# Optimization experiments

Measured on AMD Instinct MI355X. Metric: run time of the kernel, lower is better.

Reference implementation:

```python
import jax, jax.numpy as jnp
import numpy as np

N, T, C, K = 32, 1024, 512, 64
EPS = 1e-12  # torch F.normalize eps


def _l2norm(v, axis):
    n = jnp.sqrt(jnp.sum(v * v, axis=axis, keepdims=True))
    return v / jnp.maximum(n, EPS)


def setup_inputs() -> dict:
    key = jax.random.key(0)
    k1, k2 = jax.random.split(key)
    x = jax.random.normal(k1, (N, T, C), dtype=jnp.float32)
    centroids = jax.random.uniform(k2, (K, C), dtype=jnp.float32)
    # mirrors _init_params: conv.weight = 0.2*centroids, conv.bias = -0.1*||centroids||
    W = 0.2 * centroids
    b = -0.1 * jnp.sqrt(jnp.sum(centroids * centroids, axis=1))
    return {"x": x, "W": W, "b": b, "centroids": centroids}


def reference(x, W, b, centroids):
    # x: [N, T, C] -> [N, C, T]
    xt = jnp.transpose(x, (0, 2, 1))
    # 1x1 Conv1d == per-timestep linear: logits [N, K, T]
    logits = jnp.einsum('kc,nct->nkt', W, xt) + b[None, :, None]
    a = jax.nn.softmax(logits, axis=1)  # softmax over clusters
    # vlad[n,k,c] = sum_t a[n,k,t] * (x[n,c,t] - centroid[k,c])
    #            = (a @ x^T) - sum_t(a) * centroid  (GEMM form, same math)
    vlad = jnp.einsum('nkt,nct->nkc', a, xt) - a.sum(axis=-1)[:, :, None] * centroids[None]
    vlad = _l2norm(vlad, axis=2)          # intra-normalization per cluster
    vlad = vlad.reshape(vlad.shape[0], -1)
    vlad = _l2norm(vlad, axis=1)          # global L2 normalization
    return vlad
```

## Files before the change

kernel.cpp:

```cpp
#include <hip/hip_runtime.h>
#include <cmath>

namespace {

constexpr int N = 32, T = 1024, C = 512, K = 64;
constexpr float EPS = 1e-12f;

typedef short s8v __attribute__((ext_vector_type(8)));
typedef short s4v __attribute__((ext_vector_type(4)));
typedef short s2v __attribute__((ext_vector_type(2)));
typedef float f4v __attribute__((ext_vector_type(4)));

__device__ inline unsigned short f2bh(float f) {
  __bf16 h = (__bf16)f;
  return __builtin_bit_cast(unsigned short, h);
}
__device__ inline float bh2f(unsigned short u) {
  __bf16 h = __builtin_bit_cast(__bf16, u);
  return (float)h;
}

#define MFMA16(A, B, Cc) __builtin_amdgcn_mfma_f32_16x16x32_bf16((A), (B), (Cc), 0, 0, 0)

__global__ __launch_bounds__(256, 4) void k_gemm1(
    const float* __restrict__ x, const float* __restrict__ W,
    const float* __restrict__ b, float* __restrict__ aT,
    float* __restrict__ asum_part) {
  __shared__ __align__(16) unsigned short sm[4 * 64 * 72];
  __shared__ float asum_l[256];
  unsigned short* xh_s = sm;
  unsigned short* xl_s = sm + 64 * 72;
  unsigned short* wh_s = sm + 2 * 64 * 72;
  unsigned short* wl_s = sm + 3 * 64 * 72;

  const int tid = threadIdx.x;
  const int w = tid >> 6, lane = tid & 63, lm = lane & 15, lq = lane >> 4;
  const int th = w >> 1;
  const int kh = w & 1;
  const long r0 = (long)blockIdx.x * 64;
  const int n = blockIdx.x >> 4, tl = blockIdx.x & 15;

  f4v acc[2][2] = {};
  float4 px[4], pw[4];
#pragma unroll
  for (int r = 0; r < 4; ++r) {
    const int f = tid + r * 256, t = f >> 4, cg = f & 15;
    px[r] = *(const float4*)&x[(r0 + t) * C + cg * 4];
    pw[r] = *(const float4*)&W[(long)t * C + cg * 4];
  }

  for (int c0 = 0; c0 < C; c0 += 64) {
    __syncthreads();
#pragma unroll
    for (int r = 0; r < 4; ++r) {
      const int f = tid + r * 256, t = f >> 4, cg = f & 15;
      const float ex[4] = {px[r].x, px[r].y, px[r].z, px[r].w};
      const float ew[4] = {pw[r].x, pw[r].y, pw[r].z, pw[r].w};
      s4v xh, xl, wh, wl;
#pragma unroll
      for (int i = 0; i < 4; ++i) {
        unsigned short hb = f2bh(ex[i]);
        xh[i] = (short)hb; xl[i] = (short)f2bh(ex[i] - bh2f(hb));
        hb = f2bh(ew[i]);
        wh[i] = (short)hb; wl[i] = (short)f2bh(ew[i] - bh2f(hb));
      }
      *(s4v*)&xh_s[t * 72 + cg * 4] = xh;
      *(s4v*)&xl_s[t * 72 + cg * 4] = xl;
      *(s4v*)&wh_s[t * 72 + cg * 4] = wh;
      *(s4v*)&wl_s[t * 72 + cg * 4] = wl;
    }
    __syncthreads();
    if (c0 + 64 < C) {
#pragma unroll
      for (int r = 0; r < 4; ++r) {
        const int f = tid + r * 256, t = f >> 4, cg = f & 15;
        px[r] = *(const float4*)&x[(r0 + t) * C + c0 + 64 + cg * 4];
        pw[r] = *(const float4*)&W[(long)t * C + c0 + 64 + cg * 4];
      }
    }

#pragma unroll
    for (int ks = 0; ks < 2; ++ks) {
      const int col = ks * 32 + lq * 8;
      s8v ah[2], al[2], bh[2], bl[2];
#pragma unroll
      for (int i = 0; i < 2; ++i) {
        ah[i] = *(const s8v*)&xh_s[(th * 32 + i * 16 + lm) * 72 + col];
        al[i] = *(const s8v*)&xl_s[(th * 32 + i * 16 + lm) * 72 + col];
        bh[i] = *(const s8v*)&wh_s[(kh * 32 + i * 16 + lm) * 72 + col];
        bl[i] = *(const s8v*)&wl_s[(kh * 32 + i * 16 + lm) * 72 + col];
      }
#pragma unroll
      for (int i = 0; i < 2; ++i)
#pragma unroll
        for (int j = 0; j < 2; ++j) {
          acc[i][j] = MFMA16(ah[i], bh[j], acc[i][j]);
          acc[i][j] = MFMA16(ah[i], bl[j], acc[i][j]);
          acc[i][j] = MFMA16(al[i], bh[j], acc[i][j]);
        }
    }
  }
  __syncthreads();

  float* Ls = (float*)sm;
  float* Ls2 = (float*)(sm + 8704);
  const float bias[2] = {b[kh * 32 + lm], b[kh * 32 + 16 + lm]};
#pragma unroll
  for (int i = 0; i < 2; ++i)
#pragma unroll
    for (int j = 0; j < 2; ++j)
#pragma unroll
      for (int r = 0; r < 4; ++r)
        Ls[(th * 32 + i * 16 + lq * 4 + r) * 68 + kh * 32 + j * 16 + lm] =
            acc[i][j][r] + bias[j];
  __syncthreads();

  {
    const int row = tid >> 2, q = tid & 3;
    float av[16];
#pragma unroll
    for (int u = 0; u < 4; ++u)
      *(float4*)&av[u * 4] = *(const float4*)&Ls[row * 68 + q * 16 + u * 4];
    float m = av[0];
#pragma unroll
    for (int i = 1; i < 16; ++i) m = fmaxf(m, av[i]);
    m = fmaxf(m, __shfl_xor(m, 1, 64));
    m = fmaxf(m, __shfl_xor(m, 2, 64));
    float sum = 0.f;
#pragma unroll
    for (int i = 0; i < 16; ++i) {
      av[i] = __expf(av[i] - m);
      sum += av[i];
    }
    sum += __shfl_xor(sum, 1, 64);
    sum += __shfl_xor(sum, 2, 64);
    const float inv = 1.f / sum;
    float ps[16];
#pragma unroll
    for (int i = 0; i < 16; ++i) {
      av[i] *= inv;
      ps[i] = av[i];
      Ls2[(q * 16 + i) * 68 + row] = av[i];
    }
#pragma unroll
    for (int s = 4; s < 64; s <<= 1)
#pragma unroll
      for (int i = 0; i < 16; ++i) ps[i] += __shfl_xor(ps[i], s, 64);
    if (lane < 4) {
#pragma unroll
      for (int i = 0; i < 16; ++i) asum_l[w * 64 + q * 16 + i] = ps[i];
    }
  }
  __syncthreads();

  if (tid < 64) {
    asum_part[(n * 16 + tl) * 64 + tid] = asum_l[tid] + asum_l[64 + tid] +
                                          asum_l[128 + tid] + asum_l[192 + tid];
  }
#pragma unroll
  for (int r = 0; r < 4; ++r) {
    const int u = tid + r * 256, k = u >> 4, tg = u & 15;
    *(float4*)&aT[((long)n * K + k) * T + tl * 64 + tg * 4] =
        *(const float4*)&Ls2[k * 68 + tg * 4];
  }
}

__global__ __launch_bounds__(256, 4) void k_gemm2(
    const float* __restrict__ x, const float* __restrict__ aT,
    const float* __restrict__ asum_part, const float* __restrict__ cent,
    float* __restrict__ vlad, float* __restrict__ ssq_part) {
  __shared__ __align__(16) unsigned short sm[(2 * 64 + 2 * 32) * 72];
  __shared__ float asum_l[64];
  __shared__ float ssq_l[128];
  unsigned short* ah_s = sm;
  unsigned short* al_s = sm + 64 * 72;
  unsigned short* xh_s = sm + 2 * 64 * 72;
  unsigned short* xl_s = sm + 2 * 64 * 72 + 32 * 72;

  const int tid = threadIdx.x;
  const int w = tid >> 6, lane = tid & 63, lm = lane & 15, lq = lane >> 4;
  const int kh = w >> 1;
  const int ch = w & 1;
  const int p = blockIdx.x;
  const int g = p >> 3;
  const int n = ((g & 3) << 3) | (p & 7);
  const int cq = g >> 2;
  const int c0 = cq * 32;

  if (tid < 64) {
    float s = 0.f;
#pragma unroll
    for (int tl = 0; tl < 16; ++tl) s += asum_part[(n * 16 + tl) * 64 + tid];
    asum_l[tid] = s;
  }

  f4v acc[2] = {};
  float4 pa[4], px[2];
#pragma unroll
  for (int r = 0; r < 4; ++r) {
    const int u = tid + r * 256, k = u >> 4, tg = u & 15;
    pa[r] = *(const float4*)&aT[((long)n * K + k) * T + tg * 4];
  }
  {
    const int cg = tid & 7, tq = tid >> 3;
#pragma unroll
    for (int i = 0; i < 2; ++i)
      px[i] = *(const float4*)&x[((long)n * T + tq * 2 + i) * C + c0 + cg * 4];
  }

  for (int t0 = 0; t0 < T; t0 += 64) {
    __syncthreads();
#pragma unroll
    for (int r = 0; r < 4; ++r) {
      const int u = tid + r * 256, k = u >> 4, tg = u & 15;
      const float e[4] = {pa[r].x, pa[r].y, pa[r].z, pa[r].w};
      s4v h, l;
#pragma unroll
      for (int i = 0; i < 4; ++i) {
        unsigned short hb = f2bh(e[i]);
        h[i] = (short)hb;
        l[i] = (short)f2bh(e[i] - bh2f(hb));
      }
      *(s4v*)&ah_s[k * 72 + tg * 4] = h;
      *(s4v*)&al_s[k * 72 + tg * 4] = l;
    }
    {
      const int cg = tid & 7, tq = tid >> 3;
#pragma unroll
      for (int cc = 0; cc < 4; ++cc) {
        s2v h, l;
#pragma unroll
        for (int i = 0; i < 2; ++i) {
          const float e = ((const float*)&px[i])[cc];
          unsigned short hb = f2bh(e);
          h[i] = (short)hb;
          l[i] = (short)f2bh(e - bh2f(hb));
        }
        *(s2v*)&xh_s[(cg * 4 + cc) * 72 + tq * 2] = h;
        *(s2v*)&xl_s[(cg * 4 + cc) * 72 + tq * 2] = l;
      }
    }
    __syncthreads();
    if (t0 + 64 < T) {
#pragma unroll
      for (int r = 0; r < 4; ++r) {
        const int u = tid + r * 256, k = u >> 4, tg = u & 15;
        pa[r] = *(const float4*)&aT[((long)n * K + k) * T + t0 + 64 + tg * 4];
      }
      const int cg = tid & 7, tq = tid >> 3;
#pragma unroll
      for (int i = 0; i < 2; ++i)
        px[i] = *(const float4*)&x[((long)n * T + t0 + 64 + tq * 2 + i) * C +
                                   c0 + cg * 4];
    }

#pragma unroll
    for (int ks = 0; ks < 2; ++ks) {
      const int col = ks * 32 + lq * 8;
      s8v ah[2], al[2];
#pragma unroll
      for (int i = 0; i < 2; ++i) {
        ah[i] = *(const s8v*)&ah_s[(kh * 32 + i * 16 + lm) * 72 + col];
        al[i] = *(const s8v*)&al_s[(kh * 32 + i * 16 + lm) * 72 + col];
      }
      const s8v bh = *(const s8v*)&xh_s[(ch * 16 + lm) * 72 + col];
      const s8v bl = *(const s8v*)&xl_s[(ch * 16 + lm) * 72 + col];
#pragma unroll
      for (int i = 0; i < 2; ++i) {
        acc[i] = MFMA16(ah[i], bh, acc[i]);
        acc[i] = MFMA16(ah[i], bl, acc[i]);
        acc[i] = MFMA16(al[i], bh, acc[i]);
      }
    }
  }

  float ssqp[2][4];
#pragma unroll
  for (int i = 0; i < 2; ++i) {
#pragma unroll
    for (int r = 0; r < 4; ++r) {
      const int k = kh * 32 + i * 16 + lq * 4 + r;
      const float as = asum_l[k];
      const int c = c0 + ch * 16 + lm;
      const float v = acc[i][r] - as * cent[(long)k * C + c];
      vlad[((long)n * K + k) * C + c] = v;
      ssqp[i][r] = v * v;
    }
  }
#pragma unroll
  for (int i = 0; i < 2; ++i)
#pragma unroll
    for (int r = 0; r < 4; ++r) {
      float s = ssqp[i][r];
      s += __shfl_xor(s, 1, 64);
      s += __shfl_xor(s, 2, 64);
      s += __shfl_xor(s, 4, 64);
      s += __shfl_xor(s, 8, 64);
      ssqp[i][r] = s;
    }
  if (lm == 0) {
#pragma unroll
    for (int i = 0; i < 2; ++i)
#pragma unroll
      for (int r = 0; r < 4; ++r)
        ssq_l[(kh * 32 + i * 16 + lq * 4 + r) * 2 + ch] = ssqp[i][r];
  }
  __syncthreads();
  if (tid < 64)
    ssq_part[(n * 16 + cq) * 64 + tid] = ssq_l[tid * 2] + ssq_l[tid * 2 + 1];
}

__global__ __launch_bounds__(256) void k_norm(
    const float* __restrict__ vlad, const float* __restrict__ ssq_part,
    float* __restrict__ out) {
  __shared__ float denom[64];
  __shared__ float contrib[64];
  __shared__ float ginv;

  const int tid = threadIdx.x;
  const int n = blockIdx.x >> 4;
  const int chunk = blockIdx.x & 15;

  if (tid < 64) {
    float ss = 0.f;
#pragma unroll
    for (int q = 0; q < 16; ++q) ss += ssq_part[(n * 16 + q) * 64 + tid];
    const float d = fmaxf(sqrtf(ss), EPS);
    denom[tid] = d;
    contrib[tid] = ss / (d * d);
  }
  __syncthreads();
  if (tid == 0) {
    float s = 0.f;
#pragma unroll
    for (int k = 0; k < K; ++k) s += contrib[k];
    ginv = 1.0f / fmaxf(sqrtf(s), EPS);
  }
  __syncthreads();

#pragma unroll
  for (int q = 0; q < 2; ++q) {
    const int f4 = tid + q * 256;
    const long off = chunk * 2048 + (long)f4 * 4;
    const int k = (int)(off >> 9);
    float4 v = *(const float4*)&vlad[(long)n * K * C + off];
    const float sc = ginv / denom[k];
    v.x *= sc; v.y *= sc; v.z *= sc; v.w *= sc;
    *(float4*)&out[(long)n * K * C + off] = v;
  }
}

}

extern "C" void kernel_launch(void* const* d_in, const int* in_sizes, int n_in,
                              void* d_out, int out_size, void* d_ws,
                              size_t ws_size, hipStream_t stream) {
  const float* x = reinterpret_cast<const float*>(d_in[0]);
  const float* W = reinterpret_cast<const float*>(d_in[1]);
  const float* b = reinterpret_cast<const float*>(d_in[2]);
  const float* cent = reinterpret_cast<const float*>(d_in[3]);
  float* out = reinterpret_cast<float*>(d_out);

  float* p = reinterpret_cast<float*>(d_ws);
  float* aTg = p;                 p += (size_t)N * K * T;
  float* vlad = p;                p += (size_t)N * K * C;
  float* asum_part = p;           p += (size_t)512 * 64;
  float* ssq_part = p;

  k_gemm1<<<(N * T) / 64, 256, 0, stream>>>(x, W, b, aTg, asum_part);
  k_gemm2<<<N * 16, 256, 0, stream>>>(x, aTg, asum_part, cent, vlad, ssq_part);
  k_norm<<<N * 16, 256, 0, stream>>>(vlad, ssq_part, out);
}
```

Baseline: 126.3 us.

## Double threads per block in both GEMM kernels with smaller per-wave tiles

Both GEMM kernels now launch 512 threads (8 waves) instead of 256. Each wave computes half as many output tiles: gemm1 splits clusters four ways, and gemm2 splits them into 16-row slices. Load, convert and softmax loops are remapped to the larger thread count, and the x staging in gemm2 now writes single shorts. The aim is more waves in flight to hide memory latency, at the cost of more redundant LDS fragment loads per MFMA and narrower LDS stores.

```diff
diff --git a/kernel.cpp b/kernel.cpp
--- a/kernel.cpp
+++ b/kernel.cpp
@@ -8,7 +8,6 @@
 
 typedef short s8v __attribute__((ext_vector_type(8)));
 typedef short s4v __attribute__((ext_vector_type(4)));
-typedef short s2v __attribute__((ext_vector_type(2)));
 typedef float f4v __attribute__((ext_vector_type(4)));
 
 __device__ inline unsigned short f2bh(float f) {
@@ -22,12 +21,12 @@
 
 #define MFMA16(A, B, Cc) __builtin_amdgcn_mfma_f32_16x16x32_bf16((A), (B), (Cc), 0, 0, 0)
 
-__global__ __launch_bounds__(256, 4) void k_gemm1(
+__global__ __launch_bounds__(512, 4) void k_gemm1(
     const float* __restrict__ x, const float* __restrict__ W,
     const float* __restrict__ b, float* __restrict__ aT,
     float* __restrict__ asum_part) {
   __shared__ __align__(16) unsigned short sm[4 * 64 * 72];
-  __shared__ float asum_l[256];
+  __shared__ float asum_l[512];
   unsigned short* xh_s = sm;
   unsigned short* xl_s = sm + 64 * 72;
   unsigned short* wh_s = sm + 2 * 64 * 72;
@@ -35,16 +34,16 @@
 
   const int tid = threadIdx.x;
   const int w = tid >> 6, lane = tid & 63, lm = lane & 15, lq = lane >> 4;
-  const int th = w >> 1;
-  const int kh = w & 1;
+  const int th = w >> 2;
+  const int kq = w & 3;
   const long r0 = (long)blockIdx.x * 64;
   const int n = blockIdx.x >> 4, tl = blockIdx.x & 15;
 
-  f4v acc[2][2] = {};
-  float4 px[4], pw[4];
-#pragma unroll
-  for (int r = 0; r < 4; ++r) {
-    const int f = tid + r * 256, t = f >> 4, cg = f & 15;
+  f4v acc[2] = {};
+  float4 px[2], pw[2];
+#pragma unroll
+  for (int r = 0; r < 2; ++r) {
+    const int f = tid + r * 512, t = f >> 4, cg = f & 15;
     px[r] = *(const float4*)&x[(r0 + t) * C + cg * 4];
     pw[r] = *(const float4*)&W[(long)t * C + cg * 4];
   }
@@ -52,8 +51,8 @@
   for (int c0 = 0; c0 < C; c0 += 64) {
     __syncthreads();
 #pragma unroll
-    for (int r = 0; r < 4; ++r) {
-      const int f = tid + r * 256, t = f >> 4, cg = f & 15;
+    for (int r = 0; r < 2; ++r) {
+      const int f = tid + r * 512, t = f >> 4, cg = f & 15;
       const float ex[4] = {px[r].x, px[r].y, px[r].z, px[r].w};
       const float ew[4] = {pw[r].x, pw[r].y, pw[r].z, pw[r].w};
       s4v xh, xl, wh, wl;
@@ -72,8 +71,8 @@
     __syncthreads();
     if (c0 + 64 < C) {
 #pragma unroll
-      for (int r = 0; r < 4; ++r) {
-        const int f = tid + r * 256, t = f >> 4, cg = f & 15;
+      for (int r = 0; r < 2; ++r) {
+        const int f = tid + r * 512, t = f >> 4, cg = f & 15;
         px[r] = *(const float4*)&x[(r0 + t) * C + c0 + 64 + cg * 4];
         pw[r] = *(const float4*)&W[(long)t * C + c0 + 64 + cg * 4];
       }
@@ -82,90 +81,90 @@
 #pragma unroll
     for (int ks = 0; ks < 2; ++ks) {
       const int col = ks * 32 + lq * 8;
-      s8v ah[2], al[2], bh[2], bl[2];
+      s8v ah[2], al[2];
 #pragma unroll
       for (int i = 0; i < 2; ++i) {
         ah[i] = *(const s8v*)&xh_s[(th * 32 + i * 16 + lm) * 72 + col];
         al[i] = *(const s8v*)&xl_s[(th * 32 + i * 16 + lm) * 72 + col];
-        bh[i] = *(const s8v*)&wh_s[(kh * 32 + i * 16 + lm) * 72 + col];
-        bl[i] = *(const s8v*)&wl_s[(kh * 32 + i * 16 + lm) * 72 + col];
-      }
-#pragma unroll
-      for (int i = 0; i < 2; ++i)
-#pragma unroll
-        for (int j = 0; j < 2; ++j) {
-          acc[i][j] = MFMA16(ah[i], bh[j], acc[i][j]);
-          acc[i][j] = MFMA16(ah[i], bl[j], acc[i][j]);
-          acc[i][j] = MFMA16(al[i], bh[j], acc[i][j]);
-        }
+      }
+      const s8v bh = *(const s8v*)&wh_s[(kq * 16 + lm) * 72 + col];
+      const s8v bl = *(const s8v*)&wl_s[(kq * 16 + lm) * 72 + col];
+#pragma unroll
+      for (int i = 0; i < 2; ++i) {
+        acc[i] = MFMA16(ah[i], bh, acc[i]);
+        acc[i] = MFMA16(ah[i], bl, acc[i]);
+        acc[i] = MFMA16(al[i], bh, acc[i]);
+      }
     }
   }
   __syncthreads();
 
   float* Ls = (float*)sm;
-  float* Ls2 = (float*)(sm + 8704);
-  const float bias[2] = {b[kh * 32 + lm], b[kh * 32 + 16 + lm]};
+  float* Ls2 = (float*)((unsigned char*)sm + 17408);
+  const float bias = b[kq * 16 + lm];
 #pragma unroll
   for (int i = 0; i < 2; ++i)
 #pragma unroll
-    for (int j = 0; j < 2; ++j)
-#pragma unroll
-      for (int r = 0; r < 4; ++r)
-        Ls[(th * 32 + i * 16 + lq * 4 + r) * 68 + kh * 32 + j * 16 + lm] =
-            acc[i][j][r] + bias[j];
+    for (int r = 0; r < 4; ++r)
+      Ls[(th * 32 + i * 16 + lq * 4 + r) * 68 + kq * 16 + lm] =
+          acc[i][r] + bias;
   __syncthreads();
 
   {
-    const int row = tid >> 2, q = tid & 3;
-    float av[16];
-#pragma unroll
-    for (int u = 0; u < 4; ++u)
-      *(float4*)&av[u * 4] = *(const float4*)&Ls[row * 68 + q * 16 + u * 4];
+    const int row = tid >> 3, q = tid & 7;
+    float av[8];
+#pragma unroll
+    for (int u = 0; u < 2; ++u)
+      *(float4*)&av[u * 4] = *(const float4*)&Ls[row * 68 + q * 8 + u * 4];
     float m = av[0];
 #pragma unroll
-    for (int i = 1; i < 16; ++i) m = fmaxf(m, av[i]);
+    for (int i = 1; i < 8; ++i) m = fmaxf(m, av[i]);
     m = fmaxf(m, __shfl_xor(m, 1, 64));
     m = fmaxf(m, __shfl_xor(m, 2, 64));
+    m = fmaxf(m, __shfl_xor(m, 4, 64));
     float sum = 0.f;
 #pragma unroll
-    for (int i = 0; i < 16; ++i) {
+    for (int i = 0; i < 8; ++i) {
       av[i] = __expf(av[i] - m);
       sum += av[i];
     }
     sum += __shfl_xor(sum, 1, 64);
     sum += __shfl_xor(sum, 2, 64);
+    sum += __shfl_xor(sum, 4, 64);
     const float inv = 1.f / sum;
-    float ps[16];
-#pragma unroll
-    for (int i = 0; i < 16; ++i) {
+    float ps[8];
+#pragma unroll
+    for (int i = 0; i < 8; ++i) {
       av[i] *= inv;
       ps[i] = av[i];
-      Ls2[(q * 16 + i) * 68 + row] = av[i];
-    }
-#pragma unroll
-    for (int s = 4; s < 64; s <<= 1)
-#pragma unroll
-      for (int i = 0; i < 16; ++i) ps[i] += __shfl_xor(ps[i], s, 64);
-    if (lane < 4) {
-#pragma unroll
-      for (int i = 0; i < 16; ++i) asum_l[w * 64 + q * 16 + i] = ps[i];
+      Ls2[(q * 8 + i) * 68 + row] = av[i];
+    }
+#pragma unroll
+    for (int s = 8; s < 64; s <<= 1)
+#pragma unroll
+      for (int i = 0; i < 8; ++i) ps[i] += __shfl_xor(ps[i], s, 64);
+    if (lane < 8) {
+#pragma unroll
+      for (int i = 0; i < 8; ++i) asum_l[w * 64 + q * 8 + i] = ps[i];
     }
   }
   __syncthreads();
 
   if (tid < 64) {
-    asum_part[(n * 16 + tl) * 64 + tid] = asum_l[tid] + asum_l[64 + tid] +
-                                          asum_l[128 + tid] + asum_l[192 + tid];
-  }
-#pragma unroll
-  for (int r = 0; r < 4; ++r) {
-    const int u = tid + r * 256, k = u >> 4, tg = u & 15;
+    float s = 0.f;
+#pragma unroll
+    for (int j = 0; j < 8; ++j) s += asum_l[j * 64 + tid];
+    asum_part[(n * 16 + tl) * 64 + tid] = s;
+  }
+#pragma unroll
+  for (int r = 0; r < 2; ++r) {
+    const int u = tid + r * 512, k = u >> 4, tg = u & 15;
     *(float4*)&aT[((long)n * K + k) * T + tl * 64 + tg * 4] =
         *(const float4*)&Ls2[k * 68 + tg * 4];
   }
 }
 
-__global__ __launch_bounds__(256, 4) void k_gemm2(
+__global__ __launch_bounds__(512, 4) void k_gemm2(
     const float* __restrict__ x, const float* __restrict__ aT,
     const float* __restrict__ asum_part, const float* __restrict__ cent,
     float* __restrict__ vlad, float* __restrict__ ssq_part) {
@@ -194,25 +193,23 @@
     asum_l[tid] = s;
   }
 
-  f4v acc[2] = {};
-  float4 pa[4], px[2];
-#pragma unroll
-  for (int r = 0; r < 4; ++r) {
-    const int u = tid + r * 256, k = u >> 4, tg = u & 15;
+  f4v acc = {};
+  float4 pa[2], px;
+#pragma unroll
+  for (int r = 0; r < 2; ++r) {
+    const int u = tid + r * 512, k = u >> 4, tg = u & 15;
     pa[r] = *(const float4*)&aT[((long)n * K + k) * T + tg * 4];
   }
   {
     const int cg = tid & 7, tq = tid >> 3;
-#pragma unroll
-    for (int i = 0; i < 2; ++i)
-      px[i] = *(const float4*)&x[((long)n * T + tq * 2 + i) * C + c0 + cg * 4];
+    px = *(const float4*)&x[((long)n * T + tq) * C + c0 + cg * 4];
   }
 
   for (int t0 = 0; t0 < T; t0 += 64) {
     __syncthreads();
 #pragma unroll
-    for (int r = 0; r < 4; ++r) {
-      const int u = tid + r * 256, k = u >> 4, tg = u & 15;
+    for (int r = 0; r < 2; ++r) {
+      const int u = tid + r * 512, k = u >> 4, tg = u & 15;
       const float e[4] = {pa[r].x, pa[r].y, pa[r].z, pa[r].w};
       s4v h, l;
 #pragma unroll
@@ -226,84 +223,62 @@
     }
     {
       const int cg = tid & 7, tq = tid >> 3;
+      const float e4[4] = {px.x, px.y, px.z, px.w};
 #pragma unroll
       for (int cc = 0; cc < 4; ++cc) {
-        s2v h, l;
-#pragma unroll
-        for (int i = 0; i < 2; ++i) {
-          const float e = ((const float*)&px[i])[cc];
-          unsigned short hb = f2bh(e);
-          h[i] = (short)hb;
-          l[i] = (short)f2bh(e - bh2f(hb));
-        }
-        *(s2v*)&xh_s[(cg * 4 + cc) * 72 + tq * 2] = h;
-        *(s2v*)&xl_s[(cg * 4 + cc) * 72 + tq * 2] = l;
+        const float e = e4[cc];
+        const unsigned short hb = f2bh(e);
+        xh_s[(cg * 4 + cc) * 72 + tq] = hb;
+        xl_s[(cg * 4 + cc) * 72 + tq] = f2bh(e - bh2f(hb));
       }
     }
     __syncthreads();
     if (t0 + 64 < T) {
 #pragma unroll
-      for (int r = 0; r < 4; ++r) {
-        const int u = tid + r * 256, k = u >> 4, tg = u & 15;
+      for (int r = 0; r < 2; ++r) {
+        const int u = tid + r * 512, k = u >> 4, tg = u & 15;
         pa[r] = *(const float4*)&aT[((long)n * K + k) * T + t0 + 64 + tg * 4];
       }
       const int cg = tid & 7, tq = tid >> 3;
-#pragma unroll
-      for (int i = 0; i < 2; ++i)
-        px[i] = *(const float4*)&x[((long)n * T + t0 + 64 + tq * 2 + i) * C +
-                                   c0 + cg * 4];
+      px = *(const float4*)&x[((long)n * T + t0 + 64 + tq) * C + c0 + cg * 4];
     }
 
 #pragma unroll
     for (int ks = 0; ks < 2; ++ks) {
       const int col = ks * 32 + lq * 8;
-      s8v ah[2], al[2];
-#pragma unroll
-      for (int i = 0; i < 2; ++i) {
-        ah[i] = *(const s8v*)&ah_s[(kh * 32 + i * 16 + lm) * 72 + col];
-        al[i] = *(const s8v*)&al_s[(kh * 32 + i * 16 + lm) * 72 + col];
-      }
+      const s8v ah = *(const s8v*)&ah_s[(kh * 16 + lm) * 72 + col];
+      const s8v al = *(const s8v*)&al_s[(kh * 16 + lm) * 72 + col];
       const s8v bh = *(const s8v*)&xh_s[(ch * 16 + lm) * 72 + col];
       const s8v bl = *(const s8v*)&xl_s[(ch * 16 + lm) * 72 + col];
-#pragma unroll
-      for (int i = 0; i < 2; ++i) {
-        acc[i] = MFMA16(ah[i], bh, acc[i]);
-        acc[i] = MFMA16(ah[i], bl, acc[i]);
-        acc[i] = MFMA16(al[i], bh, acc[i]);
-      }
-    }
-  }
-
-  float ssqp[2][4];
-#pragma unroll
-  for (int i = 0; i < 2; ++i) {
-#pragma unroll
-    for (int r = 0; r < 4; ++r) {
-      const int k = kh * 32 + i * 16 + lq * 4 + r;
-      const float as = asum_l[k];
-      const int c = c0 + ch * 16 + lm;
-      const float v = acc[i][r] - as * cent[(long)k * C + c];
-      vlad[((long)n * K + k) * C + c] = v;
-      ssqp[i][r] = v * v;
-    }
-  }
-#pragma unroll
-  for (int i = 0; i < 2; ++i)
-#pragma unroll
-    for (int r = 0; r < 4; ++r) {
-      float s = ssqp[i][r];
-      s += __shfl_xor(s, 1, 64);
-      s += __shfl_xor(s, 2, 64);
-      s += __shfl_xor(s, 4, 64);
-      s += __shfl_xor(s, 8, 64);
-      ssqp[i][r] = s;
-    }
+      acc = MFMA16(ah, bh, acc);
+      acc = MFMA16(ah, bl, acc);
+      acc = MFMA16(al, bh, acc);
+    }
+  }
+
+  float ssqp[4];
+#pragma unroll
+  for (int r = 0; r < 4; ++r) {
+    const int k = kh * 16 + lq * 4 + r;
+    const float as = asum_l[k];
+    const int c = c0 + ch * 16 + lm;
+    const float v = acc[r] - as * cent[(long)k * C + c];
+    vlad[((long)n * K + k) * C + c] = v;
+    ssqp[r] = v * v;
+  }
+#pragma unroll
+  for (int r = 0; r < 4; ++r) {
+    float s = ssqp[r];
+    s += __shfl_xor(s, 1, 64);
+    s += __shfl_xor(s, 2, 64);
+    s += __shfl_xor(s, 4, 64);
+    s += __shfl_xor(s, 8, 64);
+    ssqp[r] = s;
+  }
   if (lm == 0) {
 #pragma unroll
-    for (int i = 0; i < 2; ++i)
-#pragma unroll
-      for (int r = 0; r < 4; ++r)
-        ssq_l[(kh * 32 + i * 16 + lq * 4 + r) * 2 + ch] = ssqp[i][r];
+    for (int r = 0; r < 4; ++r)
+      ssq_l[(kh * 16 + lq * 4 + r) * 2 + ch] = ssqp[r];
   }
   __syncthreads();
   if (tid < 64)
@@ -367,7 +342,7 @@
   float* asum_part = p;           p += (size_t)512 * 64;
   float* ssq_part = p;
 
-  k_gemm1<<<(N * T) / 64, 256, 0, stream>>>(x, W, b, aTg, asum_part);
-  k_gemm2<<<N * 16, 256, 0, stream>>>(x, aTg, asum_part, cent, vlad, ssq_part);
+  k_gemm1<<<(N * T) / 64, 512, 0, stream>>>(x, W, b, aTg, asum_part);
+  k_gemm2<<<N * 16, 512, 0, stream>>>(x, aTg, asum_part, cent, vlad, ssq_part);
   k_norm<<<N * 16, 256, 0, stream>>>(vlad, ssq_part, out);
 }
```

Result: slower. 130.9 us (+3.7%).

## Double-buffer LDS in both GEMMs and store soft-assignments as pre-split bf16 pairs

Applied to the files above, without the earlier changes.

Both GEMM kernels now use two LDS buffers so that the bf16 hi/lo split and the LDS store of the next chunk overlap the MFMA work on the current chunk. This halves the barriers per chunk and adds a second register prefetch stage. Separately, k_gemm1 now writes the softmax assignments already split into bf16 hi and lo arrays instead of fp32. k_gemm2 therefore copies them straight into LDS without converting them, at the same global byte count. LDS use per block doubles, about 73 KB in gemm1, which may reduce occupancy below the requested 4 blocks per CU.

```diff
diff --git a/kernel.cpp b/kernel.cpp
--- a/kernel.cpp
+++ b/kernel.cpp
@@ -24,14 +24,11 @@
 
 __global__ __launch_bounds__(256, 4) void k_gemm1(
     const float* __restrict__ x, const float* __restrict__ W,
-    const float* __restrict__ b, float* __restrict__ aT,
-    float* __restrict__ asum_part) {
-  __shared__ __align__(16) unsigned short sm[4 * 64 * 72];
+    const float* __restrict__ b, unsigned short* __restrict__ aTh,
+    unsigned short* __restrict__ aTl, float* __restrict__ asum_part) {
+  __shared__ __align__(16) unsigned short sm0[4 * 64 * 72];
+  __shared__ __align__(16) unsigned short sm1[4 * 64 * 72];
   __shared__ float asum_l[256];
-  unsigned short* xh_s = sm;
-  unsigned short* xl_s = sm + 64 * 72;
-  unsigned short* wh_s = sm + 2 * 64 * 72;
-  unsigned short* wl_s = sm + 3 * 64 * 72;
 
   const int tid = threadIdx.x;
   const int w = tid >> 6, lane = tid & 63, lm = lane & 15, lq = lane >> 4;
@@ -41,69 +38,86 @@
   const int n = blockIdx.x >> 4, tl = blockIdx.x & 15;
 
   f4v acc[2][2] = {};
-  float4 px[4], pw[4];
-#pragma unroll
-  for (int r = 0; r < 4; ++r) {
-    const int f = tid + r * 256, t = f >> 4, cg = f & 15;
-    px[r] = *(const float4*)&x[(r0 + t) * C + cg * 4];
-    pw[r] = *(const float4*)&W[(long)t * C + cg * 4];
-  }
-
-  for (int c0 = 0; c0 < C; c0 += 64) {
+  float4 px0[4], pw0[4], px1[4], pw1[4];
+
+#define G1_LOAD(s, c0)                                                       \
+  {                                                                          \
+    _Pragma("unroll") for (int r = 0; r < 4; ++r) {                          \
+      const int f = tid + r * 256, t = f >> 4, cg = f & 15;                  \
+      px##s[r] = *(const float4*)&x[(r0 + t) * C + (c0) + cg * 4];           \
+      pw##s[r] = *(const float4*)&W[(long)t * C + (c0) + cg * 4];            \
+    }                                                                        \
+  }
+
+#define G1_STAGE(buf, s)                                                     \
+  {                                                                          \
+    unsigned short* xh_s = (buf);                                            \
+    unsigned short* xl_s = (buf) + 64 * 72;                                  \
+    unsigned short* wh_s = (buf) + 2 * 64 * 72;                              \
+    unsigned short* wl_s = (buf) + 3 * 64 * 72;                              \
+    _Pragma("unroll") for (int r = 0; r < 4; ++r) {                          \
+      const int f = tid + r * 256, t = f >> 4, cg = f & 15;                  \
+      const float ex[4] = {px##s[r].x, px##s[r].y, px##s[r].z, px##s[r].w};  \
+      const float ew[4] = {pw##s[r].x, pw##s[r].y, pw##s[r].z, pw##s[r].w};  \
+      s4v xh, xl, wh, wl;                                                    \
+      _Pragma("unroll") for (int i = 0; i < 4; ++i) {                        \
+        unsigned short hb = f2bh(ex[i]);                                     \
+        xh[i] = (short)hb; xl[i] = (short)f2bh(ex[i] - bh2f(hb));            \
+        hb = f2bh(ew[i]);                                                    \
+        wh[i] = (short)hb; wl[i] = (short)f2bh(ew[i] - bh2f(hb));            \
+      }                                                                      \
+      *(s4v*)&xh_s[t * 72 + cg * 4] = xh;                                    \
+      *(s4v*)&xl_s[t * 72 + cg * 4] = xl;                                    \
+      *(s4v*)&wh_s[t * 72 + cg * 4] = wh;                                    \
+      *(s4v*)&wl_s[t * 72 + cg * 4] = wl;                                    \
+    }                                                                        \
+  }
+
+#define G1_MFMA(buf)                                                         \
+  {                                                                          \
+    unsigned short* xh_s = (buf);                                            \
+    unsigned short* xl_s = (buf) + 64 * 72;                                  \
+    unsigned short* wh_s = (buf) + 2 * 64 * 72;                              \
+    unsigned short* wl_s = (buf) + 3 * 64 * 72;                              \
+    _Pragma("unroll") for (int ks = 0; ks < 2; ++ks) {                       \
+      const int col = ks * 32 + lq * 8;                                      \
+      s8v ah[2], al[2], bh[2], bl[2];                                        \
+      _Pragma("unroll") for (int i = 0; i < 2; ++i) {                        \
+        ah[i] = *(const s8v*)&xh_s[(th * 32 + i * 16 + lm) * 72 + col];      \
+        al[i] = *(const s8v*)&xl_s[(th * 32 + i * 16 + lm) * 72 + col];      \
+        bh[i] = *(const s8v*)&wh_s[(kh * 32 + i * 16 + lm) * 72 + col];      \
+        bl[i] = *(const s8v*)&wl_s[(kh * 32 + i * 16 + lm) * 72 + col];      \
+      }                                                                      \
+      _Pragma("unroll") for (int i = 0; i < 2; ++i)                          \
+          _Pragma("unroll") for (int j = 0; j < 2; ++j) {                    \
+        acc[i][j] = MFMA16(ah[i], bh[j], acc[i][j]);                         \
+        acc[i][j] = MFMA16(ah[i], bl[j], acc[i][j]);                         \
+        acc[i][j] = MFMA16(al[i], bh[j], acc[i][j]);                         \
+      }                                                                      \
+    }                                                                        \
+  }
+
+  G1_LOAD(0, 0);
+  G1_STAGE(sm0, 0);
+  G1_LOAD(1, 64);
+  __syncthreads();
+  for (int c0 = 0; c0 < C; c0 += 128) {
+    if (c0 + 128 < C) G1_LOAD(0, c0 + 128);
+    G1_STAGE(sm1, 1);
+    G1_MFMA(sm0);
     __syncthreads();
-#pragma unroll
-    for (int r = 0; r < 4; ++r) {
-      const int f = tid + r * 256, t = f >> 4, cg = f & 15;
-      const float ex[4] = {px[r].x, px[r].y, px[r].z, px[r].w};
-      const float ew[4] = {pw[r].x, pw[r].y, pw[r].z, pw[r].w};
-      s4v xh, xl, wh, wl;
-#pragma unroll
-      for (int i = 0; i < 4; ++i) {
-        unsigned short hb = f2bh(ex[i]);
-        xh[i] = (short)hb; xl[i] = (short)f2bh(ex[i] - bh2f(hb));
-        hb = f2bh(ew[i]);
-        wh[i] = (short)hb; wl[i] = (short)f2bh(ew[i] - bh2f(hb));
-      }
-      *(s4v*)&xh_s[t * 72 + cg * 4] = xh;
-      *(s4v*)&xl_s[t * 72 + cg * 4] = xl;
-      *(s4v*)&wh_s[t * 72 + cg * 4] = wh;
-      *(s4v*)&wl_s[t * 72 + cg * 4] = wl;
-    }
+    if (c0 + 192 < C) G1_LOAD(1, c0 + 192);
+    if (c0 + 128 < C) G1_STAGE(sm0, 0);
+    G1_MFMA(sm1);
     __syncthreads();
-    if (c0 + 64 < C) {
-#pragma unroll
-      for (int r = 0; r < 4; ++r) {
-        const int f = tid + r * 256, t = f >> 4, cg = f & 15;
-        px[r] = *(const float4*)&x[(r0 + t) * C + c0 + 64 + cg * 4];
-        pw[r] = *(const float4*)&W[(long)t * C + c0 + 64 + cg * 4];
-      }
-    }
-
-#pragma unroll
-    for (int ks = 0; ks < 2; ++ks) {
-      const int col = ks * 32 + lq * 8;
-      s8v ah[2], al[2], bh[2], bl[2];
-#pragma unroll
-      for (int i = 0; i < 2; ++i) {
-        ah[i] = *(const s8v*)&xh_s[(th * 32 + i * 16 + lm) * 72 + col];
-        al[i] = *(const s8v*)&xl_s[(th * 32 + i * 16 + lm) * 72 + col];
-        bh[i] = *(const s8v*)&wh_s[(kh * 32 + i * 16 + lm) * 72 + col];
-        bl[i] = *(const s8v*)&wl_s[(kh * 32 + i * 16 + lm) * 72 + col];
-      }
-#pragma unroll
-      for (int i = 0; i < 2; ++i)
-#pragma unroll
-        for (int j = 0; j < 2; ++j) {
-          acc[i][j] = MFMA16(ah[i], bh[j], acc[i][j]);
-          acc[i][j] = MFMA16(ah[i], bl[j], acc[i][j]);
-          acc[i][j] = MFMA16(al[i], bh[j], acc[i][j]);
-        }
-    }
-  }
-  __syncthreads();
-
-  float* Ls = (float*)sm;
-  float* Ls2 = (float*)(sm + 8704);
+  }
+#undef G1_LOAD
+#undef G1_STAGE
+#undef G1_MFMA
+
+  float* Ls = (float*)sm0;
+  unsigned short* L2h = sm1;
+  unsigned short* L2l = sm1 + 64 * 72;
   const float bias[2] = {b[kh * 32 + lm], b[kh * 32 + 16 + lm]};
 #pragma unroll
   for (int i = 0; i < 2; ++i)
@@ -140,7 +154,9 @@
     for (int i = 0; i < 16; ++i) {
       av[i] *= inv;
       ps[i] = av[i];
-      Ls2[(q * 16 + i) * 68 + row] = av[i];
+      const unsigned short hb = f2bh(av[i]);
+      L2h[(q * 16 + i) * 72 + row] = hb;
+      L2l[(q * 16 + i) * 72 + row] = f2bh(av[i] - bh2f(hb));
     }
 #pragma unroll
     for (int s = 4; s < 64; s <<= 1)
@@ -157,25 +173,25 @@
     asum_part[(n * 16 + tl) * 64 + tid] = asum_l[tid] + asum_l[64 + tid] +
                                           asum_l[128 + tid] + asum_l[192 + tid];
   }
-#pragma unroll
-  for (int r = 0; r < 4; ++r) {
-    const int u = tid + r * 256, k = u >> 4, tg = u & 15;
-    *(float4*)&aT[((long)n * K + k) * T + tl * 64 + tg * 4] =
-        *(const float4*)&Ls2[k * 68 + tg * 4];
+  {
+    const int k = tid >> 2, tg = tid & 3;
+    const long gb = ((long)n * K + k) * T + tl * 64 + tg * 16;
+    *(s8v*)&aTh[gb] = *(const s8v*)&L2h[k * 72 + tg * 16];
+    *(s8v*)&aTh[gb + 8] = *(const s8v*)&L2h[k * 72 + tg * 16 + 8];
+    *(s8v*)&aTl[gb] = *(const s8v*)&L2l[k * 72 + tg * 16];
+    *(s8v*)&aTl[gb + 8] = *(const s8v*)&L2l[k * 72 + tg * 16 + 8];
   }
 }
 
 __global__ __launch_bounds__(256, 4) void k_gemm2(
-    const float* __restrict__ x, const float* __restrict__ aT,
+    const float* __restrict__ x, const unsigned short* __restrict__ aTh,
+    const unsigned short* __restrict__ aTl,
     const float* __restrict__ asum_part, const float* __restrict__ cent,
     float* __restrict__ vlad, float* __restrict__ ssq_part) {
-  __shared__ __align__(16) unsigned short sm[(2 * 64 + 2 * 32) * 72];
+  __shared__ __align__(16) unsigned short smA[(2 * 64 + 2 * 32) * 72];
+  __shared__ __align__(16) unsigned short smB[(2 * 64 + 2 * 32) * 72];
   __shared__ float asum_l[64];
   __shared__ float ssq_l[128];
-  unsigned short* ah_s = sm;
-  unsigned short* al_s = sm + 64 * 72;
-  unsigned short* xh_s = sm + 2 * 64 * 72;
-  unsigned short* xl_s = sm + 2 * 64 * 72 + 32 * 72;
 
   const int tid = threadIdx.x;
   const int w = tid >> 6, lane = tid & 63, lm = lane & 15, lq = lane >> 4;
@@ -195,84 +211,87 @@
   }
 
   f4v acc[2] = {};
-  float4 pa[4], px[2];
-#pragma unroll
-  for (int r = 0; r < 4; ++r) {
-    const int u = tid + r * 256, k = u >> 4, tg = u & 15;
-    pa[r] = *(const float4*)&aT[((long)n * K + k) * T + tg * 4];
-  }
-  {
-    const int cg = tid & 7, tq = tid >> 3;
-#pragma unroll
-    for (int i = 0; i < 2; ++i)
-      px[i] = *(const float4*)&x[((long)n * T + tq * 2 + i) * C + c0 + cg * 4];
-  }
-
-  for (int t0 = 0; t0 < T; t0 += 64) {
+  const int ak = tid >> 2, atg = tid & 3;
+  s8v pah0[2], pal0[2], pah1[2], pal1[2];
+  float4 px0[2], px1[2];
+
+#define G2_LOAD(s, t0)                                                       \
+  {                                                                          \
+    const long ab = ((long)n * K + ak) * T + (t0) + atg * 16;                \
+    pah##s[0] = *(const s8v*)&aTh[ab];                                       \
+    pah##s[1] = *(const s8v*)&aTh[ab + 8];                                   \
+    pal##s[0] = *(const s8v*)&aTl[ab];                                       \
+    pal##s[1] = *(const s8v*)&aTl[ab + 8];                                   \
+    const int cg = tid & 7, tq = tid >> 3;                                   \
+    _Pragma("unroll") for (int i = 0; i < 2; ++i)                            \
+        px##s[i] = *(const float4*)&x[((long)n * T + (t0) + tq * 2 + i) * C +\
+                                      c0 + cg * 4];                          \
+  }
+
+#define G2_STAGE(buf, s)                                                     \
+  {                                                                          \
+    unsigned short* ah_s = (buf);                                            \
+    unsigned short* al_s = (buf) + 64 * 72;                                  \
+    unsigned short* xh_s = (buf) + 2 * 64 * 72;                              \
+    unsigned short* xl_s = (buf) + 2 * 64 * 72 + 32 * 72;                    \
+    *(s8v*)&ah_s[ak * 72 + atg * 16] = pah##s[0];                            \
+    *(s8v*)&ah_s[ak * 72 + atg * 16 + 8] = pah##s[1];                        \
+    *(s8v*)&al_s[ak * 72 + atg * 16] = pal##s[0];                            \
+    *(s8v*)&al_s[ak * 72 + atg * 16 + 8] = pal##s[1];                        \
+    const int cg = tid & 7, tq = tid >> 3;                                   \
+    _Pragma("unroll") for (int cc = 0; cc < 4; ++cc) {                       \
+      s2v h, l;                                                              \
+      _Pragma("unroll") for (int i = 0; i < 2; ++i) {                        \
+        const float e = ((const float*)&px##s[i])[cc];                       \
+        const unsigned short hb = f2bh(e);                                   \
+        h[i] = (short)hb;                                                    \
+        l[i] = (short)f2bh(e - bh2f(hb));                                    \
+      }                                                                      \
+      *(s2v*)&xh_s[(cg * 4 + cc) * 72 + tq * 2] = h;                         \
+      *(s2v*)&xl_s[(cg * 4 + cc) * 72 + tq * 2] = l;                         \
+    }                                                                        \
+  }
+
+#define G2_MFMA(buf)                                                         \
+  {                                                                          \
+    unsigned short* ah_s = (buf);                                            \
+    unsigned short* al_s = (buf) + 64 * 72;                                  \
+    unsigned short* xh_s = (buf) + 2 * 64 * 72;                              \
+    unsigned short* xl_s = (buf) + 2 * 64 * 72 + 32 * 72;                    \
+    _Pragma("unroll") for (int ks = 0; ks < 2; ++ks) {                       \
+      const int col = ks * 32 + lq * 8;                                      \
+      s8v ah[2], al[2];                                                      \
+      _Pragma("unroll") for (int i = 0; i < 2; ++i) {                        \
+        ah[i] = *(const s8v*)&ah_s[(kh * 32 + i * 16 + lm) * 72 + col];      \
+        al[i] = *(const s8v*)&al_s[(kh * 32 + i * 16 + lm) * 72 + col];      \
+      }                                                                      \
+      const s8v bh = *(const s8v*)&xh_s[(ch * 16 + lm) * 72 + col];          \
+      const s8v bl = *(const s8v*)&xl_s[(ch * 16 + lm) * 72 + col];          \
+      _Pragma("unroll") for (int i = 0; i < 2; ++i) {                        \
+        acc[i] = MFMA16(ah[i], bh, acc[i]);                                  \
+        acc[i] = MFMA16(ah[i], bl, acc[i]);                                  \
+        acc[i] = MFMA16(al[i], bh, acc[i]);                                  \
+      }                                                                      \
+    }                                                                        \
+  }
+
+  G2_LOAD(0, 0);
+  G2_STAGE(smA, 0);
+  G2_LOAD(1, 64);
+  __syncthreads();
+  for (int t0 = 0; t0 < T; t0 += 128) {
+    if (t0 + 128 < T) G2_LOAD(0, t0 + 128);
+    G2_STAGE(smB, 1);
+    G2_MFMA(smA);
     __syncthreads();
-#pragma unroll
-    for (int r = 0; r < 4; ++r) {
-      const int u = tid + r * 256, k = u >> 4, tg = u & 15;
-      const float e[4] = {pa[r].x, pa[r].y, pa[r].z, pa[r].w};
-      s4v h, l;
-#pragma unroll
-      for (int i = 0; i < 4; ++i) {
-        unsigned short hb = f2bh(e[i]);
-        h[i] = (short)hb;
-        l[i] = (short)f2bh(e[i] - bh2f(hb));
-      }
-      *(s4v*)&ah_s[k * 72 + tg * 4] = h;
-      *(s4v*)&al_s[k * 72 + tg * 4] = l;
-    }
-    {
-      const int cg = tid & 7, tq = tid >> 3;
-#pragma unroll
-      for (int cc = 0; cc < 4; ++cc) {
-        s2v h, l;
-#pragma unroll
-        for (int i = 0; i < 2; ++i) {
-          const float e = ((const float*)&px[i])[cc];
-          unsigned short hb = f2bh(e);
-          h[i] = (short)hb;
-          l[i] = (short)f2bh(e - bh2f(hb));
-        }
-        *(s2v*)&xh_s[(cg * 4 + cc) * 72 + tq * 2] = h;
-        *(s2v*)&xl_s[(cg * 4 + cc) * 72 + tq * 2] = l;
-      }
-    }
+    if (t0 + 192 < T) G2_LOAD(1, t0 + 192);
+    if (t0 + 128 < T) G2_STAGE(smA, 0);
+    G2_MFMA(smB);
     __syncthreads();
-    if (t0 + 64 < T) {
-#pragma unroll
-      for (int r = 0; r < 4; ++r) {
-        const int u = tid + r * 256, k = u >> 4, tg = u & 15;
-        pa[r] = *(const float4*)&aT[((long)n * K + k) * T + t0 + 64 + tg * 4];
-      }
-      const int cg = tid & 7, tq = tid >> 3;
-#pragma unroll
-      for (int i = 0; i < 2; ++i)
-        px[i] = *(const float4*)&x[((long)n * T + t0 + 64 + tq * 2 + i) * C +
-                                   c0 + cg * 4];
-    }
-
-#pragma unroll
-    for (int ks = 0; ks < 2; ++ks) {
-      const int col = ks * 32 + lq * 8;
-      s8v ah[2], al[2];
-#pragma unroll
-      for (int i = 0; i < 2; ++i) {
-        ah[i] = *(const s8v*)&ah_s[(kh * 32 + i * 16 + lm) * 72 + col];
-        al[i] = *(const s8v*)&al_s[(kh * 32 + i * 16 + lm) * 72 + col];
-      }
-      const s8v bh = *(const s8v*)&xh_s[(ch * 16 + lm) * 72 + col];
-      const s8v bl = *(const s8v*)&xl_s[(ch * 16 + lm) * 72 + col];
-#pragma unroll
-      for (int i = 0; i < 2; ++i) {
-        acc[i] = MFMA16(ah[i], bh, acc[i]);
-        acc[i] = MFMA16(ah[i], bl, acc[i]);
-        acc[i] = MFMA16(al[i], bh, acc[i]);
-      }
-    }
-  }
+  }
+#undef G2_LOAD
+#undef G2_STAGE
+#undef G2_MFMA
 
   float ssqp[2][4];
 #pragma unroll
@@ -361,13 +380,19 @@
   const float* cent = reinterpret_cast<const float*>(d_in[3]);
   float* out = reinterpret_cast<float*>(d_out);
 
-  float* p = reinterpret_cast<float*>(d_ws);
-  float* aTg = p;                 p += (size_t)N * K * T;
-  float* vlad = p;                p += (size_t)N * K * C;
-  float* asum_part = p;           p += (size_t)512 * 64;
-  float* ssq_part = p;
-
-  k_gemm1<<<(N * T) / 64, 256, 0, stream>>>(x, W, b, aTg, asum_part);
-  k_gemm2<<<N * 16, 256, 0, stream>>>(x, aTg, asum_part, cent, vlad, ssq_part);
+  char* pp = reinterpret_cast<char*>(d_ws);
+  unsigned short* aTh = reinterpret_cast<unsigned short*>(pp);
+  pp += (size_t)N * K * T * sizeof(unsigned short);
+  unsigned short* aTl = reinterpret_cast<unsigned short*>(pp);
+  pp += (size_t)N * K * T * sizeof(unsigned short);
+  float* vlad = reinterpret_cast<float*>(pp);
+  pp += (size_t)N * K * C * sizeof(float);
+  float* asum_part = reinterpret_cast<float*>(pp);
+  pp += (size_t)512 * 64 * sizeof(float);
+  float* ssq_part = reinterpret_cast<float*>(pp);
+
+  k_gemm1<<<(N * T) / 64, 256, 0, stream>>>(x, W, b, aTh, aTl, asum_part);
+  k_gemm2<<<N * 16, 256, 0, stream>>>(x, aTh, aTl, asum_part, cent, vlad,
+                                      ssq_part);
   k_norm<<<N * 16, 256, 0, stream>>>(vlad, ssq_part, out);
 }
```

Result: no change. 127.3 us (+0.8%).
